# Kernel tuning notes

Hardware: AMD Instinct MI355X
Metric: run time of the kernel (lower is better)

## Reference

```python
import jax, jax.numpy as jnp
import numpy as np

B, S, D = 8, 2048, 1024

def setup_inputs() -> dict:
    key = jax.random.key(0)
    ks = jax.random.split(key, 7)
    x = jax.random.normal(ks[0], (B, S, D), dtype=jnp.float32)
    s = 1.0 / np.sqrt(D)
    Wq = jax.random.normal(ks[1], (D, D), dtype=jnp.float32) * s
    bq = jax.random.normal(ks[2], (D,), dtype=jnp.float32) * 0.01
    Wk = jax.random.normal(ks[3], (D, D), dtype=jnp.float32) * s
    bk = jax.random.normal(ks[4], (D,), dtype=jnp.float32) * 0.01
    Wv = jax.random.normal(ks[5], (D, D), dtype=jnp.float32) * s
    bv = jax.random.normal(ks[6], (D,), dtype=jnp.float32) * 0.01
    return {"x": x, "Wq": Wq, "bq": bq, "Wk": Wk, "bk": bk, "Wv": Wv, "bv": bv}

def reference(x, Wq, bq, Wk, bk, Wv, bv):
    # QKV projections: [B,S,D]
    Q = jnp.einsum('bsd,de->bse', x, Wq) + bq
    K = jnp.einsum('bsd,de->bse', x, Wk) + bk
    V = jnp.einsum('bsd,de->bse', x, Wv) + bv
    scale = 1.0 / jnp.sqrt(jnp.asarray(Q.shape[-1], Q.dtype))
    attn = jnp.einsum('bqd,bkd->bqk', Q, K) * scale  # [B,S,S]
    attn = jax.nn.softmax(attn, axis=-1)
    return jnp.einsum('bqk,bkd->bqd', attn, V)
```

## Files before the change

### kernel.cpp

```cpp
#include <hip/hip_runtime.h>
#include <hip/hip_bf16.h>
#include <cstdint>


#define Bb 8
#define Ss 2048
#define Dd 1024

typedef unsigned short ushort_t;
typedef __attribute__((ext_vector_type(8))) short short8;
typedef __attribute__((ext_vector_type(4))) float floatx4;

__device__ inline ushort_t f2bf(float f) {
    unsigned int u = __float_as_uint(f);
    unsigned int r = (u + 0x7fffu + ((u >> 16) & 1u)) >> 16;
    return (ushort_t)r;
}
__device__ inline float bf2f(ushort_t u) {
    return __uint_as_float(((unsigned int)u) << 16);
}

__device__ inline floatx4 mfma16(short8 a, short8 b, floatx4 c) {
    return __builtin_amdgcn_mfma_f32_16x16x32_bf16(a, b, c, 0, 0, 0);
}

__device__ inline void gload_lds16(const void* g, void* l) {
    __builtin_amdgcn_global_load_lds(
        (const __attribute__((address_space(1))) void*)g,
        (__attribute__((address_space(3))) void*)l, 16, 0, 0);
}

__device__ __attribute__((always_inline)) void gemm_core(
    const ushort_t* __restrict__ A, const ushort_t* __restrict__ B,
    int K, int lda, int ldb, int m0, int n0, int tid,
    ushort_t* As, ushort_t* Bs, floatx4 acc[4][4])
{
    const int lane = tid & 63;
    const int wave = tid >> 6;
    const int mloc = lane & 15;
    const int q    = lane >> 4;
    const int wm   = (wave & 1) * 64;
    const int wn   = (wave >> 1) * 64;

    const int srow = lane >> 3;
    const int cg   = (lane & 7) ^ srow;
    const ushort_t* aBase = A + (size_t)(m0 + wave * 32 + srow) * lda + cg * 8;
    const ushort_t* bBase = B + (size_t)(n0 + wave * 32 + srow) * ldb + cg * 8;

    int offA[4][2], offB[4][2];
#pragma unroll
    for (int t = 0; t < 4; t++) {
        const int rA = wm + t * 16 + mloc;
        const int rB = wn + t * 16 + mloc;
#pragma unroll
        for (int h = 0; h < 2; h++) {
            offA[t][h] = rA * 64 + (((q + h * 4) ^ (rA & 7)) * 8);
            offB[t][h] = rB * 64 + (((q + h * 4) ^ (rB & 7)) * 8);
        }
    }

    for (int kt = 0; kt < K; kt += 64) {
#pragma unroll
        for (int j = 0; j < 4; j++) {
            gload_lds16(aBase + (size_t)j * 8 * lda + kt, &As[(wave * 4 + j) * 512]);
            gload_lds16(bBase + (size_t)j * 8 * ldb + kt, &Bs[(wave * 4 + j) * 512]);
        }
        __syncthreads();
#pragma unroll
        for (int h = 0; h < 2; h++) {
            short8 aF[4], bF[4];
#pragma unroll
            for (int t = 0; t < 4; t++) aF[t] = *(const short8*)&As[offA[t][h]];
#pragma unroll
            for (int t = 0; t < 4; t++) bF[t] = *(const short8*)&Bs[offB[t][h]];
#pragma unroll
            for (int mt = 0; mt < 4; mt++)
#pragma unroll
                for (int nt = 0; nt < 4; nt++)
                    acc[mt][nt] = mfma16(aF[mt], bF[nt], acc[mt][nt]);
        }
        __syncthreads();
    }
}

template <int EPI>
__global__ __launch_bounds__(256) void gemm_nt(
    const ushort_t* __restrict__ A, const ushort_t* __restrict__ B,
    void* __restrict__ Cv, const float* __restrict__ aux,
    int K, int lda, int ldb, int ldc,
    size_t strideA, size_t strideB, size_t strideC)
{
    const int z = blockIdx.z;
    A += (size_t)z * strideA;
    B += (size_t)z * strideB;
    const int m0 = blockIdx.y * 128;
    const int n0 = blockIdx.x * 128;

    __shared__ __align__(16) ushort_t As[128 * 64];
    __shared__ __align__(16) ushort_t Bs[128 * 64];

    const int tid  = threadIdx.x;
    const int lane = tid & 63;
    const int wave = tid >> 6;
    const int mloc = lane & 15;
    const int q    = lane >> 4;
    const int wm   = (wave & 1) * 64;
    const int wn   = (wave >> 1) * 64;

    floatx4 acc[4][4] = {};
    gemm_core(A, B, K, lda, ldb, m0, n0, tid, As, Bs, acc);

    if (EPI == 0) {
        ushort_t* Cb = (ushort_t*)Cv;
#pragma unroll
        for (int nt = 0; nt < 4; nt++) {
            const int gc = n0 + wn + nt * 16 + mloc;
            const float bval = aux[gc];
#pragma unroll
            for (int mt = 0; mt < 4; mt++)
#pragma unroll
                for (int r = 0; r < 4; r++) {
                    const int gr = m0 + wm + mt * 16 + q * 4 + r;
                    Cb[(size_t)gr * ldc + gc] = f2bf(acc[mt][nt][r] + bval);
                }
        }
    } else {
        float* Cf = (float*)Cv + (size_t)z * strideC;
        float iv[4][4];
#pragma unroll
        for (int mt = 0; mt < 4; mt++)
#pragma unroll
            for (int r = 0; r < 4; r++) {
                const int gr = m0 + wm + mt * 16 + q * 4 + r;
                iv[mt][r] = 1.0f / aux[z * Ss + gr];
            }
#pragma unroll
        for (int nt = 0; nt < 4; nt++) {
            const int gc = n0 + wn + nt * 16 + mloc;
#pragma unroll
            for (int mt = 0; mt < 4; mt++)
#pragma unroll
                for (int r = 0; r < 4; r++) {
                    const int gr = m0 + wm + mt * 16 + q * 4 + r;
                    Cf[(size_t)gr * ldc + gc] = acc[mt][nt][r] * iv[mt][r];
                }
        }
    }
}

__global__ __launch_bounds__(256) void score_vt(
    const ushort_t* __restrict__ QKVb, ushort_t* __restrict__ Pb,
    ushort_t* __restrict__ Vt, float* __restrict__ lsum)
{
    __shared__ __align__(16) ushort_t As[128 * 64];
    __shared__ __align__(16) ushort_t Bs[128 * 64];
    const int bid = blockIdx.x;
    const int tid = threadIdx.x;

    if (bid < 2048) {
        const int nb = bid & 15, mb = (bid >> 4) & 15, z = bid >> 8;
        const int m0 = mb * 128, n0 = nb * 128;
        const ushort_t* A = QKVb + (size_t)z * Ss * 3072;
        const ushort_t* B = A + 1024;

        floatx4 acc[4][4] = {};
        gemm_core(A, B, Dd, 3072, 3072, m0, n0, tid, As, Bs, acc);

        const int lane = tid & 63, wave = tid >> 6;
        const int mloc = lane & 15, q = lane >> 4;
        const int wm = (wave & 1) * 64, wn = (wave >> 1) * 64;
        ushort_t* Cp = Pb + (size_t)z * Ss * Ss;

        float rs[4][4] = {};
#pragma unroll
        for (int nt = 0; nt < 4; nt++) {
            const int gc = n0 + wn + nt * 16 + mloc;
#pragma unroll
            for (int mt = 0; mt < 4; mt++)
#pragma unroll
                for (int r = 0; r < 4; r++) {
                    const int gr = m0 + wm + mt * 16 + q * 4 + r;
                    const ushort_t o = f2bf(__expf(acc[mt][nt][r] * 0.03125f));
                    Cp[(size_t)gr * Ss + gc] = o;
                    rs[mt][r] += bf2f(o);
                }
        }
#pragma unroll
        for (int mt = 0; mt < 4; mt++)
#pragma unroll
            for (int r = 0; r < 4; r++) {
                float s = rs[mt][r];
                s += __shfl_xor(s, 1);
                s += __shfl_xor(s, 2);
                s += __shfl_xor(s, 4);
                s += __shfl_xor(s, 8);
                rs[mt][r] = s;
            }
        if (mloc == 0) {
#pragma unroll
            for (int mt = 0; mt < 4; mt++)
#pragma unroll
                for (int r = 0; r < 4; r++) {
                    const int gr = m0 + wm + mt * 16 + q * 4 + r;
                    atomicAdd(&lsum[z * Ss + gr], rs[mt][r]);
                }
        }
    } else {
        const int t = bid - 2048;
        const int z = t >> 9, rem = t & 511;
        const int d0 = (rem & 15) * 64, s0 = (rem >> 4) * 64;
        ushort_t (*tile)[72] = (ushort_t(*)[72])As;
        const int rr = tid >> 3;
        const int c8 = (tid & 7) * 8;
#pragma unroll
        for (int i = 0; i < 2; i++) {
            const int s = s0 + rr + i * 32;
            uint4 v = *(const uint4*)&QKVb[((size_t)(z * Ss + s)) * 3072 + 2048 + d0 + c8];
            *(uint4*)&tile[rr + i * 32][c8] = v;
        }
        __syncthreads();
#pragma unroll
        for (int i = 0; i < 2; i++) {
            const int d = rr + i * 32;
            ushort_t u[8];
#pragma unroll
            for (int j = 0; j < 8; j++) u[j] = tile[c8 + j][d];
            *(uint4*)&Vt[(size_t)z * Dd * Ss + (size_t)(d0 + d) * Ss + s0 + c8] =
                *(const uint4*)u;
        }
    }
}

__global__ __launch_bounds__(256) void prep(
    const float* __restrict__ x,
    const float* __restrict__ W0, const float* __restrict__ W1,
    const float* __restrict__ W2,
    const float* __restrict__ bq, const float* __restrict__ bk,
    const float* __restrict__ bv,
    ushort_t* __restrict__ xb, ushort_t* __restrict__ Wall,
    float* __restrict__ ball)
{
    const int bid = blockIdx.x;
    const int tid = threadIdx.x;

    if (bid < 8192) {
        const size_t i = (size_t)bid * 256 + tid;
        const float4* p = (const float4*)x + i * 2;
        float4 a = p[0], b = p[1];
        ushort_t u[8];
        u[0]=f2bf(a.x); u[1]=f2bf(a.y); u[2]=f2bf(a.z); u[3]=f2bf(a.w);
        u[4]=f2bf(b.x); u[5]=f2bf(b.y); u[6]=f2bf(b.z); u[7]=f2bf(b.w);
        *(uint4*)(xb + i * 8) = *(const uint4*)u;
    } else if (bid < 8960) {
        const int t = bid - 8192;
        const int z = t >> 8;
        const float* W = (z == 0) ? W0 : (z == 1) ? W1 : W2;
        ushort_t* Wt = Wall + (size_t)z * Dd * Dd;
        __shared__ float tt[64][65];
        const int n0 = ((t >> 4) & 15) * 64, k0 = (t & 15) * 64;
        const int r  = tid >> 4;
        const int c4 = (tid & 15) * 4;
#pragma unroll
        for (int i = 0; i < 4; i++) {
            float4 v = *(const float4*)&W[(size_t)(k0 + r + i * 16) * Dd + n0 + c4];
            tt[r + i * 16][c4 + 0] = v.x;
            tt[r + i * 16][c4 + 1] = v.y;
            tt[r + i * 16][c4 + 2] = v.z;
            tt[r + i * 16][c4 + 3] = v.w;
        }
        __syncthreads();
#pragma unroll
        for (int i = 0; i < 4; i++) {
            const int rn = r + i * 16;
            ushort_t u[4];
#pragma unroll
            for (int j = 0; j < 4; j++) u[j] = f2bf(tt[c4 + j][rn]);
            *(uint2*)&Wt[(size_t)(n0 + rn) * Dd + k0 + c4] = *(const uint2*)u;
        }
    } else {
#pragma unroll
        for (int j = 0; j < 12; j++) {
            const int idx = j * 256 + tid;
            float v = (idx < 1024) ? bq[idx]
                    : (idx < 2048) ? bk[idx - 1024] : bv[idx - 2048];
            ball[idx] = v;
        }
    }
}

extern "C" void kernel_launch(void* const* d_in, const int* in_sizes, int n_in,
                              void* d_out, int out_size, void* d_ws, size_t ws_size,
                              hipStream_t stream)
{
    const float* x  = (const float*)d_in[0];
    const float* Wq = (const float*)d_in[1];
    const float* bq = (const float*)d_in[2];
    const float* Wk = (const float*)d_in[3];
    const float* bk = (const float*)d_in[4];
    const float* Wv = (const float*)d_in[5];
    const float* bv = (const float*)d_in[6];
    float* out = (float*)d_out;

    char* ws = (char*)d_ws;
    const size_t MB = 1u << 20;
    ushort_t* xb   = (ushort_t*)(ws);
    ushort_t* Vt   = (ushort_t*)(ws);
    ushort_t* QKVb = (ushort_t*)(ws + 32 * MB);
    ushort_t* Pb   = (ushort_t*)(ws + 128 * MB);
    float*    lsum = (float*)(ws + 192 * MB);
    ushort_t* Wall = (ushort_t*)d_out;
    float*    ball = (float*)((char*)d_out + 6 * MB);

    prep<<<8961, 256, 0, stream>>>(x, Wq, Wk, Wv, bq, bk, bv, xb, Wall, ball);

    dim3 g1(3072 / 128, (Bb * Ss) / 128, 1);
    gemm_nt<0><<<g1, 256, 0, stream>>>(xb, Wall, QKVb, ball,
                                       Dd, Dd, Dd, 3072, 0, 0, 0);

    hipMemsetAsync(lsum, 0, (size_t)Bb * Ss * sizeof(float), stream);
    score_vt<<<6144, 256, 0, stream>>>(QKVb, Pb, Vt, lsum);

    dim3 g3(Dd / 128, Ss / 128, Bb);
    gemm_nt<3><<<g3, 256, 0, stream>>>(Pb, Vt, out, lsum,
                                       Ss, Ss, Ss, Dd,
                                       (size_t)Ss * Ss, (size_t)Dd * Ss,
                                       (size_t)Ss * Dd);
}
```

Before: 451.5 us.

## Switch GEMMs to 32x32x16 MFMA with 128x256 block tiles

Replaces the 16x16x32 bf16 MFMA core with the 32x32x16 variant and widens each block's N tile from 128 to 256, so each wave computes a 64x128 sub-tile. LDS traffic per MFMA drops and the larger tile gives more reuse of A and B. The epilogues and the row-sum reduction are rewritten for the 32x32 accumulator layout, and launch grids are halved in N. The cost is doubled B-tile LDS, more accumulator registers and fewer blocks, which risks lower occupancy and worse wave-count balance.

```diff
diff --git a/kernel.cpp b/kernel.cpp
--- a/kernel.cpp
+++ b/kernel.cpp
@@ -9,7 +9,7 @@
 
 typedef unsigned short ushort_t;
 typedef __attribute__((ext_vector_type(8))) short short8;
-typedef __attribute__((ext_vector_type(4))) float floatx4;
+typedef __attribute__((ext_vector_type(16))) float floatx16;
 
 __device__ inline ushort_t f2bf(float f) {
     unsigned int u = __float_as_uint(f);
@@ -20,8 +20,8 @@
     return __uint_as_float(((unsigned int)u) << 16);
 }
 
-__device__ inline floatx4 mfma16(short8 a, short8 b, floatx4 c) {
-    return __builtin_amdgcn_mfma_f32_16x16x32_bf16(a, b, c, 0, 0, 0);
+__device__ inline floatx16 mfma32(short8 a, short8 b, floatx16 c) {
+    return __builtin_amdgcn_mfma_f32_32x32x16_bf16(a, b, c, 0, 0, 0);
 }
 
 __device__ inline void gload_lds16(const void* g, void* l) {
@@ -30,61 +30,63 @@
         (__attribute__((address_space(3))) void*)l, 16, 0, 0);
 }
 
-__device__ __attribute__((always_inline)) void gemm_core(
+__device__ __attribute__((always_inline)) void gemm_core32(
     const ushort_t* __restrict__ A, const ushort_t* __restrict__ B,
     int K, int lda, int ldb, int m0, int n0, int tid,
-    ushort_t* As, ushort_t* Bs, floatx4 acc[4][4])
+    ushort_t* As, ushort_t* Bs, floatx16 acc[2][4])
 {
     const int lane = tid & 63;
     const int wave = tid >> 6;
-    const int mloc = lane & 15;
-    const int q    = lane >> 4;
+    const int nloc = lane & 31;
+    const int h    = lane >> 5;
     const int wm   = (wave & 1) * 64;
-    const int wn   = (wave >> 1) * 64;
+    const int wn   = (wave >> 1) * 128;
 
     const int srow = lane >> 3;
     const int cg   = (lane & 7) ^ srow;
     const ushort_t* aBase = A + (size_t)(m0 + wave * 32 + srow) * lda + cg * 8;
-    const ushort_t* bBase = B + (size_t)(n0 + wave * 32 + srow) * ldb + cg * 8;
-
-    int offA[4][2], offB[4][2];
-#pragma unroll
-    for (int t = 0; t < 4; t++) {
-        const int rA = wm + t * 16 + mloc;
-        const int rB = wn + t * 16 + mloc;
-#pragma unroll
-        for (int h = 0; h < 2; h++) {
-            offA[t][h] = rA * 64 + (((q + h * 4) ^ (rA & 7)) * 8);
-            offB[t][h] = rB * 64 + (((q + h * 4) ^ (rB & 7)) * 8);
-        }
-    }
+    const ushort_t* bBase = B + (size_t)(n0 + wave * 64 + srow) * ldb + cg * 8;
+
+    int rowA[2], rowB[4];
+#pragma unroll
+    for (int mt = 0; mt < 2; mt++) rowA[mt] = (wm + mt * 32 + nloc) * 64;
+#pragma unroll
+    for (int nt = 0; nt < 4; nt++) rowB[nt] = (wn + nt * 32 + nloc) * 64;
+    const int xr = lane & 7;
 
     for (int kt = 0; kt < K; kt += 64) {
 #pragma unroll
-        for (int j = 0; j < 4; j++) {
+        for (int j = 0; j < 4; j++)
             gload_lds16(aBase + (size_t)j * 8 * lda + kt, &As[(wave * 4 + j) * 512]);
-            gload_lds16(bBase + (size_t)j * 8 * ldb + kt, &Bs[(wave * 4 + j) * 512]);
-        }
+#pragma unroll
+        for (int j = 0; j < 8; j++)
+            gload_lds16(bBase + (size_t)j * 8 * ldb + kt, &Bs[(wave * 8 + j) * 512]);
         __syncthreads();
-#pragma unroll
-        for (int h = 0; h < 2; h++) {
-            short8 aF[4], bF[4];
-#pragma unroll
-            for (int t = 0; t < 4; t++) aF[t] = *(const short8*)&As[offA[t][h]];
-#pragma unroll
-            for (int t = 0; t < 4; t++) bF[t] = *(const short8*)&Bs[offB[t][h]];
-#pragma unroll
-            for (int mt = 0; mt < 4; mt++)
+
+#pragma unroll
+        for (int step = 0; step < 4; step++) {
+            const int pos = (((step * 2 + h) ^ xr) * 8);
+            short8 aF[2], bF[4];
+#pragma unroll
+            for (int mt = 0; mt < 2; mt++)
+                aF[mt] = *(const short8*)&As[rowA[mt] + pos];
+#pragma unroll
+            for (int nt = 0; nt < 4; nt++)
+                bF[nt] = *(const short8*)&Bs[rowB[nt] + pos];
+#pragma unroll
+            for (int mt = 0; mt < 2; mt++)
 #pragma unroll
                 for (int nt = 0; nt < 4; nt++)
-                    acc[mt][nt] = mfma16(aF[mt], bF[nt], acc[mt][nt]);
+                    acc[mt][nt] = mfma32(aF[mt], bF[nt], acc[mt][nt]);
         }
         __syncthreads();
     }
 }
 
+#define CD_ROW(reg, h) (((reg) & 3) + 8 * ((reg) >> 2) + 4 * (h))
+
 template <int EPI>
-__global__ __launch_bounds__(256) void gemm_nt(
+__global__ __launch_bounds__(256, 2) void gemm_nt(
     const ushort_t* __restrict__ A, const ushort_t* __restrict__ B,
     void* __restrict__ Cv, const float* __restrict__ aux,
     int K, int lda, int ldb, int ldc,
@@ -94,119 +96,113 @@
     A += (size_t)z * strideA;
     B += (size_t)z * strideB;
     const int m0 = blockIdx.y * 128;
-    const int n0 = blockIdx.x * 128;
+    const int n0 = blockIdx.x * 256;
 
     __shared__ __align__(16) ushort_t As[128 * 64];
-    __shared__ __align__(16) ushort_t Bs[128 * 64];
+    __shared__ __align__(16) ushort_t Bs[256 * 64];
 
     const int tid  = threadIdx.x;
     const int lane = tid & 63;
     const int wave = tid >> 6;
-    const int mloc = lane & 15;
-    const int q    = lane >> 4;
+    const int nloc = lane & 31;
+    const int h    = lane >> 5;
     const int wm   = (wave & 1) * 64;
-    const int wn   = (wave >> 1) * 64;
-
-    floatx4 acc[4][4] = {};
-    gemm_core(A, B, K, lda, ldb, m0, n0, tid, As, Bs, acc);
+    const int wn   = (wave >> 1) * 128;
+
+    floatx16 acc[2][4] = {};
+    gemm_core32(A, B, K, lda, ldb, m0, n0, tid, As, Bs, acc);
 
     if (EPI == 0) {
         ushort_t* Cb = (ushort_t*)Cv;
 #pragma unroll
         for (int nt = 0; nt < 4; nt++) {
-            const int gc = n0 + wn + nt * 16 + mloc;
+            const int gc = n0 + wn + nt * 32 + nloc;
             const float bval = aux[gc];
 #pragma unroll
-            for (int mt = 0; mt < 4; mt++)
-#pragma unroll
-                for (int r = 0; r < 4; r++) {
-                    const int gr = m0 + wm + mt * 16 + q * 4 + r;
-                    Cb[(size_t)gr * ldc + gc] = f2bf(acc[mt][nt][r] + bval);
+            for (int mt = 0; mt < 2; mt++)
+#pragma unroll
+                for (int reg = 0; reg < 16; reg++) {
+                    const int gr = m0 + wm + mt * 32 + CD_ROW(reg, h);
+                    Cb[(size_t)gr * ldc + gc] = f2bf(acc[mt][nt][reg] + bval);
                 }
         }
     } else {
         float* Cf = (float*)Cv + (size_t)z * strideC;
-        float iv[4][4];
-#pragma unroll
-        for (int mt = 0; mt < 4; mt++)
-#pragma unroll
-            for (int r = 0; r < 4; r++) {
-                const int gr = m0 + wm + mt * 16 + q * 4 + r;
-                iv[mt][r] = 1.0f / aux[z * Ss + gr];
+#pragma unroll
+        for (int mt = 0; mt < 2; mt++)
+#pragma unroll
+            for (int reg = 0; reg < 16; reg++) {
+                const int gr = m0 + wm + mt * 32 + CD_ROW(reg, h);
+                const float iv = 1.0f / aux[z * Ss + gr];
+#pragma unroll
+                for (int nt = 0; nt < 4; nt++) {
+                    const int gc = n0 + wn + nt * 32 + nloc;
+                    Cf[(size_t)gr * ldc + gc] = acc[mt][nt][reg] * iv;
+                }
             }
-#pragma unroll
-        for (int nt = 0; nt < 4; nt++) {
-            const int gc = n0 + wn + nt * 16 + mloc;
-#pragma unroll
-            for (int mt = 0; mt < 4; mt++)
-#pragma unroll
-                for (int r = 0; r < 4; r++) {
-                    const int gr = m0 + wm + mt * 16 + q * 4 + r;
-                    Cf[(size_t)gr * ldc + gc] = acc[mt][nt][r] * iv[mt][r];
-                }
-        }
     }
 }
 
-__global__ __launch_bounds__(256) void score_vt(
+__global__ __launch_bounds__(256, 2) void score_vt(
     const ushort_t* __restrict__ QKVb, ushort_t* __restrict__ Pb,
     ushort_t* __restrict__ Vt, float* __restrict__ lsum)
 {
     __shared__ __align__(16) ushort_t As[128 * 64];
-    __shared__ __align__(16) ushort_t Bs[128 * 64];
+    __shared__ __align__(16) ushort_t Bs[256 * 64];
     const int bid = blockIdx.x;
     const int tid = threadIdx.x;
 
-    if (bid < 2048) {
-        const int nb = bid & 15, mb = (bid >> 4) & 15, z = bid >> 8;
-        const int m0 = mb * 128, n0 = nb * 128;
+    if (bid < 1024) {
+        const int nb = bid & 7, mb = (bid >> 3) & 15, z = bid >> 7;
+        const int m0 = mb * 128, n0 = nb * 256;
         const ushort_t* A = QKVb + (size_t)z * Ss * 3072;
         const ushort_t* B = A + 1024;
 
-        floatx4 acc[4][4] = {};
-        gemm_core(A, B, Dd, 3072, 3072, m0, n0, tid, As, Bs, acc);
+        floatx16 acc[2][4] = {};
+        gemm_core32(A, B, Dd, 3072, 3072, m0, n0, tid, As, Bs, acc);
 
         const int lane = tid & 63, wave = tid >> 6;
-        const int mloc = lane & 15, q = lane >> 4;
-        const int wm = (wave & 1) * 64, wn = (wave >> 1) * 64;
+        const int nloc = lane & 31, h = lane >> 5;
+        const int wm = (wave & 1) * 64, wn = (wave >> 1) * 128;
         ushort_t* Cp = Pb + (size_t)z * Ss * Ss;
 
-        float rs[4][4] = {};
+        float rs[2][16] = {};
 #pragma unroll
         for (int nt = 0; nt < 4; nt++) {
-            const int gc = n0 + wn + nt * 16 + mloc;
-#pragma unroll
-            for (int mt = 0; mt < 4; mt++)
-#pragma unroll
-                for (int r = 0; r < 4; r++) {
-                    const int gr = m0 + wm + mt * 16 + q * 4 + r;
-                    const ushort_t o = f2bf(__expf(acc[mt][nt][r] * 0.03125f));
+            const int gc = n0 + wn + nt * 32 + nloc;
+#pragma unroll
+            for (int mt = 0; mt < 2; mt++)
+#pragma unroll
+                for (int reg = 0; reg < 16; reg++) {
+                    const int gr = m0 + wm + mt * 32 + CD_ROW(reg, h);
+                    const ushort_t o = f2bf(__expf(acc[mt][nt][reg] * 0.03125f));
                     Cp[(size_t)gr * Ss + gc] = o;
-                    rs[mt][r] += bf2f(o);
+                    rs[mt][reg] += bf2f(o);
                 }
         }
 #pragma unroll
-        for (int mt = 0; mt < 4; mt++)
-#pragma unroll
-            for (int r = 0; r < 4; r++) {
-                float s = rs[mt][r];
+        for (int mt = 0; mt < 2; mt++)
+#pragma unroll
+            for (int reg = 0; reg < 16; reg++) {
+                float s = rs[mt][reg];
                 s += __shfl_xor(s, 1);
                 s += __shfl_xor(s, 2);
                 s += __shfl_xor(s, 4);
                 s += __shfl_xor(s, 8);
-                rs[mt][r] = s;
+                s += __shfl_xor(s, 16);
+                rs[mt][reg] = s;
             }
-        if (mloc == 0) {
-#pragma unroll
-            for (int mt = 0; mt < 4; mt++)
-#pragma unroll
-                for (int r = 0; r < 4; r++) {
-                    const int gr = m0 + wm + mt * 16 + q * 4 + r;
-                    atomicAdd(&lsum[z * Ss + gr], rs[mt][r]);
+        if (nloc == 0) {
+#pragma unroll
+            for (int mt = 0; mt < 2; mt++)
+#pragma unroll
+                for (int reg = 0; reg < 16; reg++) {
+                    const int gr = m0 + wm + mt * 32 + CD_ROW(reg, h);
+                    atomicAdd(&lsum[z * Ss + gr], rs[mt][reg]);
                 }
         }
     } else {
-        const int t = bid - 2048;
+        const int t = bid - 1024;
         const int z = t >> 9, rem = t & 511;
         const int d0 = (rem & 15) * 64, s0 = (rem >> 4) * 64;
         ushort_t (*tile)[72] = (ushort_t(*)[72])As;
@@ -313,14 +309,14 @@
 
     prep<<<8961, 256, 0, stream>>>(x, Wq, Wk, Wv, bq, bk, bv, xb, Wall, ball);
 
-    dim3 g1(3072 / 128, (Bb * Ss) / 128, 1);
+    dim3 g1(3072 / 256, (Bb * Ss) / 128, 1);
     gemm_nt<0><<<g1, 256, 0, stream>>>(xb, Wall, QKVb, ball,
                                        Dd, Dd, Dd, 3072, 0, 0, 0);
 
     hipMemsetAsync(lsum, 0, (size_t)Bb * Ss * sizeof(float), stream);
-    score_vt<<<6144, 256, 0, stream>>>(QKVb, Pb, Vt, lsum);
-
-    dim3 g3(Dd / 128, Ss / 128, Bb);
+    score_vt<<<5120, 256, 0, stream>>>(QKVb, Pb, Vt, lsum);
+
+    dim3 g3(Dd / 256, Ss / 128, Bb);
     gemm_nt<3><<<g3, 256, 0, stream>>>(Pb, Vt, out, lsum,
                                        Ss, Ss, Ss, Dd,
                                        (size_t)Ss * Ss, (size_t)Dd * Ss,
```

After: 398.0 us. -11.8%, faster.
